# Kernel tuning notes

Measured on AMD Instinct MI355X. Metric: run time of the kernel, lower is better.

The kernel has to match this reference:

```python
import jax, jax.numpy as jnp
import numpy as np

N_NODES = 20000
N_EDGES = 320000
L = 512   # input feature dim (size_dict['small'][0])
D = 256   # hidden dim (feat_channel), heads=1 so head_dim = 256
C = 2     # n_classes


def setup_inputs() -> dict:
    key = jax.random.key(0)
    ks = jax.random.split(key, 18)
    s = 0.02
    inp = {
        "x": jax.random.normal(ks[0], (N_NODES, L), jnp.float32),
        "edge_index": jax.random.randint(ks[1], (2, N_EDGES), 0, N_NODES, dtype=jnp.int32),
        "label": 1,
        # TransformerConv(L, D, heads=1): query/key/value + root skip projections
        "Wq": jax.random.normal(ks[2], (L, D), jnp.float32) * s,
        "bq": jax.random.normal(ks[3], (D,), jnp.float32) * s,
        "Wk": jax.random.normal(ks[4], (L, D), jnp.float32) * s,
        "bk": jax.random.normal(ks[5], (D,), jnp.float32) * s,
        "Wv": jax.random.normal(ks[6], (L, D), jnp.float32) * s,
        "bv": jax.random.normal(ks[7], (D,), jnp.float32) * s,
        "Ws": jax.random.normal(ks[8], (L, D), jnp.float32) * s,
        "bs": jax.random.normal(ks[9], (D,), jnp.float32) * s,
        # GlobalAdaptPooling: tanh-MLP attention (heads = n_classes) + per-class classifier
        "Wa1": jax.random.normal(ks[10], (D, D), jnp.float32) * s,
        "ba1": jax.random.normal(ks[11], (D,), jnp.float32) * s,
        "Wa2": jax.random.normal(ks[12], (D, C), jnp.float32) * s,
        "ba2": jax.random.normal(ks[13], (C,), jnp.float32) * s,
        "Wc": jax.random.normal(ks[14], (C, D), jnp.float32) * s,
        "bc": jax.random.normal(ks[15], (C,), jnp.float32) * s,
    }
    return inp


def _forward(x, edge_index, label, Wq, bq, Wk, bk, Wv, bv, Ws, bs, Wa1, ba1, Wa2, ba2, Wc, bc):
    n = x.shape[0]
    src = edge_index[0]  # message source j
    dst = edge_index[1]  # message target i
    # --- TransformerConv (heads=1, concat, root_weight=True) ---
    q = x @ Wq + bq                      # [N, D]
    k = x @ Wk + bk
    v = x @ Wv + bv
    score = jnp.sum(q[dst] * k[src], axis=-1) / jnp.sqrt(jnp.float32(D))  # [E]
    # segment softmax over incoming edges of each target node
    m = jax.ops.segment_max(score, dst, num_segments=n)
    e = jnp.exp(score - m[dst])
    den = jax.ops.segment_sum(e, dst, num_segments=n)
    alpha = e / den[dst]                 # [E]
    agg = jax.ops.segment_sum(alpha[:, None] * v[src], dst, num_segments=n)  # [N, D]
    h = agg + x @ Ws + bs
    # --- act: GELU (torch exact/erf) ---
    h = jax.nn.gelu(h, approximate=False)
    # --- GlobalAdaptPooling: node attention with n_classes heads ---
    scores = jnp.tanh(h @ Wa1 + ba1) @ Wa2 + ba2      # [N, C]
    attn = jax.nn.softmax(scores, axis=0)             # softmax over nodes
    M = attn.T @ h                                    # [C, D] per-class bag embedding
    logits = (jnp.sum(M * Wc, axis=1) + bc)[None, :]  # [1, C]
    Y_prob = jax.nn.softmax(logits, axis=1)
    A = attn[:, label]                                # [N] attention for target class
    return logits, Y_prob, A


def reference(x, edge_index, label, Wq, bq, Wk, bk, Wv, bv, Ws, bs, Wa1, ba1, Wa2, ba2, Wc, bc):
    return _forward(x, edge_index, label, Wq, bq, Wk, bk, Wv, bv, Ws, bs, Wa1, ba1, Wa2, ba2, Wc, bc)
```

## Files before the change

kernel.cpp:

```cpp
#include <hip/hip_runtime.h>
#include <hip/hip_bf16.h>
#include <math.h>

typedef float f32x4_t __attribute__((ext_vector_type(4)));
typedef float f32x2_t __attribute__((ext_vector_type(2)));
typedef __bf16 bf16x8_t __attribute__((ext_vector_type(8)));

__device__ __forceinline__ float bf2f(unsigned int u){
  union { float f; unsigned int i; } x; x.i = u << 16; return x.f;
}
__device__ __forceinline__ unsigned short f2bf(float f){
  unsigned int x = __float_as_uint(f);
  unsigned int r = (x + 0x7fffu + ((x >> 16) & 1u)) >> 16;
  return (unsigned short)r;
}
__device__ __forceinline__ unsigned int pk2bf(float a, float b){
  return (unsigned int)f2bf(a) | ((unsigned int)f2bf(b) << 16);
}
__device__ __forceinline__ int swz4(int r){ return (r ^ (r >> 2) ^ (r >> 4)) & 3; }

__device__ __forceinline__ void unp8s(uint4 w, float* f, float s){
  f[0] = bf2f(w.x & 0xffffu) * s; f[1] = bf2f(w.x >> 16) * s;
  f[2] = bf2f(w.y & 0xffffu) * s; f[3] = bf2f(w.y >> 16) * s;
  f[4] = bf2f(w.z & 0xffffu) * s; f[5] = bf2f(w.z >> 16) * s;
  f[6] = bf2f(w.w & 0xffffu) * s; f[7] = bf2f(w.w >> 16) * s;
}
__device__ __forceinline__ void unpf8(unsigned int w, float* f){
  f32x2_t lo = __builtin_amdgcn_cvt_pk_f32_fp8(w, false);
  f32x2_t hi = __builtin_amdgcn_cvt_pk_f32_fp8(w, true);
  f[0] = lo[0]; f[1] = lo[1]; f[2] = hi[0]; f[3] = hi[1];
}

#define GLOAD16(gsrc, ldst) \
  __builtin_amdgcn_global_load_lds((const __attribute__((address_space(1))) unsigned int*)(gsrc), \
                                   (__attribute__((address_space(3))) unsigned int*)(ldst), 16, 0, 0)

__global__ void zero_buf(uint4* __restrict__ p, int n16){
  int i = blockIdx.x * 256 + threadIdx.x;
  if (i < n16) p[i] = make_uint4(0, 0, 0, 0);
}

__global__ void prep(const float* __restrict__ x,
                     const float* __restrict__ Wq, const float* __restrict__ Wk,
                     const float* __restrict__ Wv, const float* __restrict__ Ws,
                     const float* __restrict__ bq, const float* __restrict__ bk,
                     const float* __restrict__ bv, const float* __restrict__ bs,
                     const float* __restrict__ Wa1, const int* __restrict__ ei,
                     unsigned short* __restrict__ xbf, unsigned short* __restrict__ wcatT,
                     float* __restrict__ bcat, unsigned short* __restrict__ wa1T,
                     int* __restrict__ deg, int n, int ne, int nbcv){
  const int b = blockIdx.x, tid = threadIdx.x;
  if (b < 2048){
    int idx = b * 256 + tid;
    int c = idx >> 9, k = idx & 511;
    int sel = c >> 8, cc = c & 255;
    const float* W = (sel == 0) ? Wq : (sel == 1) ? Wk : (sel == 2) ? Wv : Ws;
    int p = ((k >> 3) & 3) ^ swz4(c & 127);
    int dst = c * 512 + (k & ~31) + p * 8 + (k & 7);
    wcatT[dst] = f2bf(W[k * 256 + cc]);
    if (idx < 1024){
      int sel2 = idx >> 8, cc2 = idx & 255;
      const float* B = (sel2 == 0) ? bq : (sel2 == 1) ? bk : (sel2 == 2) ? bv : bs;
      bcat[idx] = B[cc2];
    }
  } else if (b < 2304){
    int idx = (b - 2048) * 256 + tid;
    int c = idx >> 8, k = idx & 255;
    wa1T[idx] = f2bf(Wa1[k * 256 + c]);
  } else if (b < 2304 + nbcv){
    int idx = (b - 2304) * 256 + tid;
    if (idx < n * 64){
      int node = idx >> 6, un = idx & 63;
      int k0 = (un >> 2) * 32, u = un & 3;
      const float* src = x + (size_t)node * 512 + k0 + u * 8;
      float4 f0 = *reinterpret_cast<const float4*>(src);
      float4 f1 = *reinterpret_cast<const float4*>(src + 4);
      uint4 o;
      o.x = pk2bf(f0.x, f0.y); o.y = pk2bf(f0.z, f0.w);
      o.z = pk2bf(f1.x, f1.y); o.w = pk2bf(f1.z, f1.w);
      int p = u ^ swz4(node & 127);
      *reinterpret_cast<uint4*>(xbf + (size_t)node * 512 + k0 + p * 8) = o;
    }
  } else {
    int i = (b - 2304 - nbcv) * 256 + tid;
    if (i < ne) atomicAdd(&deg[ei[ne + i]], 1);
  }
}

__global__ __launch_bounds__(256) void gemm_qkvs(const unsigned short* __restrict__ xbf,
                                                 const unsigned short* __restrict__ wcatT,
                                                 const float* __restrict__ bcat,
                                                 unsigned short* __restrict__ qbf,
                                                 unsigned short* __restrict__ sbf,
                                                 unsigned char* __restrict__ kv8,
                                                 int n_nodes, int mblocks){
  __shared__ __align__(16) unsigned char smem[49152];
  const int tid = threadIdx.x;
  const int lane = tid & 63, wave = tid >> 6;
  const int wm = wave >> 1, wn = wave & 1;
  const int g = (blockIdx.x & 7) * mblocks + (blockIdx.x >> 3);
  const int m_blk = g >> 3, n_blk = g & 7;
  const int m0 = m_blk * 128, n0 = n_blk * 128;
  const int lrow = lane >> 2;
  const int lcol = (lane & 3) * 8;
  const int rA0 = min(m0 + wave * 16 + lrow, n_nodes - 1);
  const int rA1 = min(m0 + (wave + 4) * 16 + lrow, n_nodes - 1);
  const int rB0 = n0 + wave * 16 + lrow;
  const int rB1 = rB0 + 64;
  const int r = lane & 15, q4 = lane >> 4;
  const unsigned short* aG0 = xbf   + (size_t)rA0 * 512 + lcol;
  const unsigned short* aG1 = xbf   + (size_t)rA1 * 512 + lcol;
  const unsigned short* bG0 = wcatT + (size_t)rB0 * 512 + lcol;
  const unsigned short* bG1 = wcatT + (size_t)rB1 * 512 + lcol;
  int aoff[4], boff[4];
  #pragma unroll
  for (int mi = 0; mi < 4; mi++){ int rr = wm * 64 + mi * 16 + r; aoff[mi] = rr * 32 + ((q4 ^ swz4(rr)) * 8); }
  #pragma unroll
  for (int ni = 0; ni < 4; ni++){ int rb = wn * 64 + ni * 16 + r; boff[ni] = rb * 32 + ((q4 ^ swz4(rb)) * 8); }
  f32x4_t acc[4][4] = {};
#define STAGE(base, k0) { \
    unsigned short* As_ = (unsigned short*)(smem + (base)); \
    unsigned short* Bs_ = (unsigned short*)(smem + (base) + 8192); \
    GLOAD16(aG0 + (k0), &As_[wave * 512]); \
    GLOAD16(aG1 + (k0), &As_[(wave + 4) * 512]); \
    GLOAD16(bG0 + (k0), &Bs_[wave * 512]); \
    GLOAD16(bG1 + (k0), &Bs_[(wave + 4) * 512]); \
  }
  STAGE(0, 0);
  STAGE(16384, 32);
  int cbase = 0;
  int sbase = 32768;
  for (int t = 0; t < 16; t++){
    if (t + 2 < 16){
      STAGE(sbase, (t + 2) * 32);
      asm volatile("s_waitcnt vmcnt(8)" ::: "memory");
    } else if (t + 1 < 16){
      asm volatile("s_waitcnt vmcnt(4)" ::: "memory");
    } else {
      asm volatile("s_waitcnt vmcnt(0)" ::: "memory");
    }
    __builtin_amdgcn_s_barrier();
    asm volatile("" ::: "memory");
    const unsigned short* As = (const unsigned short*)(smem + cbase);
    const unsigned short* Bs = (const unsigned short*)(smem + cbase + 8192);
    bf16x8_t a[4], b[4];
    #pragma unroll
    for (int mi = 0; mi < 4; mi++) a[mi] = *reinterpret_cast<const bf16x8_t*>(&As[aoff[mi]]);
    #pragma unroll
    for (int ni = 0; ni < 4; ni++) b[ni] = *reinterpret_cast<const bf16x8_t*>(&Bs[boff[ni]]);
    #pragma unroll
    for (int mi = 0; mi < 4; mi++)
      #pragma unroll
      for (int ni = 0; ni < 4; ni++)
        acc[mi][ni] = __builtin_amdgcn_mfma_f32_16x16x32_bf16(b[ni], a[mi], acc[mi][ni], 0, 0, 0);
    __builtin_amdgcn_s_barrier();
    asm volatile("" ::: "memory");
    cbase += 16384; if (cbase == 49152) cbase = 0;
    sbase += 16384; if (sbase == 49152) sbase = 0;
  }
#undef STAGE
  const bool isQ = (n_blk < 2), isS = (n_blk >= 6);
  if (isQ || isS){
    unsigned short* St = (unsigned short*)smem;
    unsigned short* outp = isQ ? qbf : sbf;
    const int colhalf = isQ ? n_blk : (n_blk - 6);
    #pragma unroll
    for (int ch = 0; ch < 2; ch++){
      if (wm == ch){
        #pragma unroll
        for (int mi = 0; mi < 4; mi++){
          #pragma unroll
          for (int ni = 0; ni < 4; ni++){
            int mloc = mi * 16 + r;
            int nl = wn * 64 + ni * 16 + q4 * 4;
            float4 bb = *reinterpret_cast<const float4*>(&bcat[n0 + nl]);
            uint2 w;
            w.x = pk2bf(acc[mi][ni][0] + bb.x, acc[mi][ni][1] + bb.y);
            w.y = pk2bf(acc[mi][ni][2] + bb.z, acc[mi][ni][3] + bb.w);
            *reinterpret_cast<uint2*>(&St[mloc * 152 + nl]) = w;
          }
        }
      }
      __syncthreads();
      #pragma unroll
      for (int it = 0; it < 4; it++){
        int u = it * 256 + tid;
        int row = u >> 4, seg = (u & 15) * 8;
        int node = m0 + ch * 64 + row;
        if (node < n_nodes){
          uint4 v = *reinterpret_cast<const uint4*>(&St[row * 152 + seg]);
          *reinterpret_cast<uint4*>(outp + (size_t)node * 256 + colhalf * 128 + seg) = v;
        }
      }
      __syncthreads();
    }
  } else {
    unsigned char* St8 = smem;
    #pragma unroll
    for (int ch = 0; ch < 2; ch++){
      if (wm == ch){
        #pragma unroll
        for (int mi = 0; mi < 4; mi++){
          #pragma unroll
          for (int ni = 0; ni < 4; ni++){
            int mloc = mi * 16 + r;
            int nl = wn * 64 + ni * 16 + q4 * 4;
            float4 bb = *reinterpret_cast<const float4*>(&bcat[n0 + nl]);
            int u = 0;
            u = __builtin_amdgcn_cvt_pk_fp8_f32(acc[mi][ni][0] + bb.x, acc[mi][ni][1] + bb.y, u, false);
            u = __builtin_amdgcn_cvt_pk_fp8_f32(acc[mi][ni][2] + bb.z, acc[mi][ni][3] + bb.w, u, true);
            *reinterpret_cast<unsigned int*>(&St8[mloc * 144 + nl]) = (unsigned int)u;
          }
        }
      }
      __syncthreads();
      #pragma unroll
      for (int it = 0; it < 2; it++){
        int u = it * 256 + tid;
        int row = u >> 3, seg = (u & 7) * 16;
        int node = m0 + ch * 64 + row;
        if (node < n_nodes){
          uint4 v = *reinterpret_cast<const uint4*>(&St8[row * 144 + seg]);
          *reinterpret_cast<uint4*>(kv8 + (size_t)node * 512 + (n_blk - 2) * 128 + seg) = v;
        }
      }
      __syncthreads();
    }
  }
}

__global__ void scan_deg(const int* __restrict__ deg, int* __restrict__ rowstart, int n, int ne){
  __shared__ int sm[1024];
  int tid = threadIdx.x;
  int per = (n + 1023) / 1024;
  int start = tid * per;
  int sum = 0;
  for (int i = 0; i < per; i++){
    int idx = start + i;
    sum += (idx < n) ? deg[idx] : 0;
  }
  sm[tid] = sum; __syncthreads();
  for (int off = 1; off < 1024; off <<= 1){
    int t = (tid >= off) ? sm[tid - off] : 0;
    __syncthreads();
    sm[tid] += t;
    __syncthreads();
  }
  int run = sm[tid] - sum;
  for (int i = 0; i < per; i++){
    int idx = start + i;
    if (idx < n){
      rowstart[idx] = run;
      run += deg[idx];
    }
  }
  if (tid == 0) rowstart[n] = ne;
}

__global__ void scatter_edges(const int* __restrict__ ei, const int* __restrict__ rowstart,
                              int* __restrict__ cursor, int* __restrict__ csrsrc, int ne){
  int i = blockIdx.x * 256 + threadIdx.x;
  if (i < ne){
    int d = ei[ne + i];
    int pos = atomicAdd(&cursor[d], 1);
    csrsrc[rowstart[d] + pos] = ei[i] << 9;
  }
}

__global__ __launch_bounds__(256) void edge_attn(const unsigned short* __restrict__ qbf,
                                                 const unsigned short* __restrict__ sbf,
                                                 const unsigned char* __restrict__ kv8,
                                                 const int* __restrict__ rowstart,
                                                 const int* __restrict__ csrsrc,
                                                 unsigned short* __restrict__ hbf, int n_nodes){
  const int tid = threadIdx.x;
  const int lane = tid & 63, wave = tid >> 6;
  const int g = lane >> 4, t = lane & 15;
  const int chain = g;
  const int node = blockIdx.x * 4 + wave;
  const bool active = node < n_nodes;
  const int nd = active ? node : 0;
  const float qs = 0.0625f * 1.44269504088896340736f;
  float q[16];
  {
    const unsigned short* qp = qbf + (size_t)nd * 256 + t * 16;
    uint4 w0 = *reinterpret_cast<const uint4*>(qp);
    uint4 w1 = *reinterpret_cast<const uint4*>(qp + 8);
    unp8s(w0, q, qs); unp8s(w1, q + 8, qs);
  }
  int rs = rowstart[nd];
  int re = active ? rowstart[nd + 1] : rs;
  float m = -1e30f, den = 0.f;
  float acc[16];
  #pragma unroll
  for (int j = 0; j < 16; j++) acc[j] = 0.f;
  const int i0 = rs + chain;
  uint4 kA = make_uint4(0,0,0,0), vA = kA, kB = kA, vB = kA;
  if (i0 < re){
    const unsigned char* p1 = kv8 + (size_t)csrsrc[i0] + t * 16;
    kA = *reinterpret_cast<const uint4*>(p1);
    vA = *reinterpret_cast<const uint4*>(p1 + 256);
    if (i0 + 4 < re){
      const unsigned char* p2 = kv8 + (size_t)csrsrc[i0 + 4] + t * 16;
      kB = *reinterpret_cast<const uint4*>(p2);
      vB = *reinterpret_cast<const uint4*>(p2 + 256);
    }
  }
  for (int i = i0; i < re; i += 8){
    uint4 k1 = kA, v1 = vA, k2 = kB, v2 = vB;
    const bool has2 = (i + 4 < re);
    if (i + 8 < re){
      const unsigned char* p1 = kv8 + (size_t)csrsrc[i + 8] + t * 16;
      kA = *reinterpret_cast<const uint4*>(p1);
      vA = *reinterpret_cast<const uint4*>(p1 + 256);
      if (i + 12 < re){
        const unsigned char* p2 = kv8 + (size_t)csrsrc[i + 12] + t * 16;
        kB = *reinterpret_cast<const uint4*>(p2);
        vB = *reinterpret_cast<const uint4*>(p2 + 256);
      }
    }
    float kf1[16], kf2[16];
    unpf8(k1.x, kf1); unpf8(k1.y, kf1 + 4); unpf8(k1.z, kf1 + 8); unpf8(k1.w, kf1 + 12);
    unpf8(k2.x, kf2); unpf8(k2.y, kf2 + 4); unpf8(k2.z, kf2 + 8); unpf8(k2.w, kf2 + 12);
    float s1 = 0.f, s2 = 0.f;
    #pragma unroll
    for (int j = 0; j < 16; j++){ s1 = fmaf(q[j], kf1[j], s1); s2 = fmaf(q[j], kf2[j], s2); }
    s1 += __shfl_xor(s1, 1); s2 += __shfl_xor(s2, 1);
    s1 += __shfl_xor(s1, 2); s2 += __shfl_xor(s2, 2);
    s1 += __shfl_xor(s1, 4); s2 += __shfl_xor(s2, 4);
    s1 += __shfl_xor(s1, 8); s2 += __shfl_xor(s2, 8);
    if (!has2) s2 = -1e30f;
    float vf1[16], vf2[16];
    unpf8(v1.x, vf1); unpf8(v1.y, vf1 + 4); unpf8(v1.z, vf1 + 8); unpf8(v1.w, vf1 + 12);
    unpf8(v2.x, vf2); unpf8(v2.y, vf2 + 4); unpf8(v2.z, vf2 + 8); unpf8(v2.w, vf2 + 12);
    float mn = fmaxf(m, fmaxf(s1, s2));
    float sc = exp2f(m - mn);
    float e1 = exp2f(s1 - mn);
    float e2 = exp2f(s2 - mn);
    den = den * sc + e1 + e2;
    #pragma unroll
    for (int j = 0; j < 16; j++)
      acc[j] = fmaf(acc[j], sc, fmaf(e1, vf1[j], e2 * vf2[j]));
    m = mn;
  }
  #pragma unroll
  for (int step = 16; step <= 32; step <<= 1){
    float mo  = __shfl_xor(m, step);
    float dno = __shfl_xor(den, step);
    float mn  = fmaxf(m, mo);
    float a_  = exp2f(m - mn);
    float b_  = exp2f(mo - mn);
    den = den * a_ + dno * b_;
    #pragma unroll
    for (int j = 0; j < 16; j++){
      float oth = __shfl_xor(acc[j], step);
      acc[j] = acc[j] * a_ + oth * b_;
    }
    m = mn;
  }
  float inv = (den > 0.f) ? 1.f / den : 0.f;
  const unsigned short* sp = sbf + (size_t)nd * 256 + t * 16;
  uint4 s0 = *reinterpret_cast<const uint4*>(sp);
  uint4 s1v = *reinterpret_cast<const uint4*>(sp + 8);
  float sf[16]; unp8s(s0, sf, 1.0f); unp8s(s1v, sf + 8, 1.0f);
  const float inv_sqrt2 = 0.70710678118654752f;
  unsigned int o[8];
  #pragma unroll
  for (int j = 0; j < 8; j++){
    float h0 = acc[2 * j] * inv + sf[2 * j];
    float h1 = acc[2 * j + 1] * inv + sf[2 * j + 1];
    h0 = 0.5f * h0 * (1.f + erff(h0 * inv_sqrt2));
    h1 = 0.5f * h1 * (1.f + erff(h1 * inv_sqrt2));
    o[j] = (unsigned int)f2bf(h0) | ((unsigned int)f2bf(h1) << 16);
  }
  if (active && g == 0){
    uint4* dst = reinterpret_cast<uint4*>(hbf + (size_t)node * 256 + t * 16);
    dst[0] = make_uint4(o[0], o[1], o[2], o[3]);
    dst[1] = make_uint4(o[4], o[5], o[6], o[7]);
  }
}

__global__ __launch_bounds__(256) void mlp_mfma(const unsigned short* __restrict__ hbf,
                                                const unsigned short* __restrict__ wa1T,
                                                const float* __restrict__ ba1,
                                                const float* __restrict__ Wa2,
                                                const float* __restrict__ ba2,
                                                float* __restrict__ s2, int n_nodes){
  __shared__ __align__(16) unsigned short As[64 * 72];
  __shared__ float s2s[64][2];
  const int tid = threadIdx.x;
  const int lane = tid & 63, wave = tid >> 6;
  const int m0 = blockIdx.x * 64;
  const int c0 = wave * 64;
  const int r = lane & 15, rg = (lane >> 4) * 4;
  if (tid < 128) s2s[tid >> 1][tid & 1] = 0.f;
  f32x4_t acc[4][4] = {};
  for (int k0 = 0; k0 < 256; k0 += 64){
    int arow = tid >> 2, akc = (tid & 3) * 16;
    uint4 a0v = make_uint4(0,0,0,0), a1v = make_uint4(0,0,0,0);
    if (m0 + arow < n_nodes){
      const unsigned short* src = hbf + (size_t)(m0 + arow) * 256 + k0 + akc;
      a0v = *reinterpret_cast<const uint4*>(src);
      a1v = *reinterpret_cast<const uint4*>(src + 8);
    }
    *reinterpret_cast<uint4*>(&As[arow * 72 + akc]) = a0v;
    *reinterpret_cast<uint4*>(&As[arow * 72 + akc + 8]) = a1v;
    __syncthreads();
    #pragma unroll
    for (int kk = 0; kk < 2; kk++){
      int kg = kk * 32 + (lane >> 4) * 8;
      bf16x8_t a[4], b[4];
      #pragma unroll
      for (int mi = 0; mi < 4; mi++)
        a[mi] = *reinterpret_cast<const bf16x8_t*>(&As[(mi * 16 + r) * 72 + kg]);
      #pragma unroll
      for (int ni = 0; ni < 4; ni++)
        b[ni] = *reinterpret_cast<const bf16x8_t*>(wa1T + (size_t)(c0 + ni * 16 + r) * 256 + k0 + kg);
      #pragma unroll
      for (int mi = 0; mi < 4; mi++)
        #pragma unroll
        for (int ni = 0; ni < 4; ni++)
          acc[mi][ni] = __builtin_amdgcn_mfma_f32_16x16x32_bf16(a[mi], b[ni], acc[mi][ni], 0, 0, 0);
    }
    __syncthreads();
  }
  float w20[4], w21[4], b1c[4];
  #pragma unroll
  for (int ni = 0; ni < 4; ni++){
    int col = c0 + ni * 16 + r;
    w20[ni] = Wa2[col * 2]; w21[ni] = Wa2[col * 2 + 1]; b1c[ni] = ba1[col];
  }
  #pragma unroll
  for (int mi = 0; mi < 4; mi++){
    #pragma unroll
    for (int j = 0; j < 4; j++){
      float t0 = 0.f, t1 = 0.f;
      #pragma unroll
      for (int ni = 0; ni < 4; ni++){
        float t = tanhf(acc[mi][ni][j] + b1c[ni]);
        t0 += t * w20[ni]; t1 += t * w21[ni];
      }
      t0 += __shfl_xor(t0, 1); t0 += __shfl_xor(t0, 2);
      t0 += __shfl_xor(t0, 4); t0 += __shfl_xor(t0, 8);
      t1 += __shfl_xor(t1, 1); t1 += __shfl_xor(t1, 2);
      t1 += __shfl_xor(t1, 4); t1 += __shfl_xor(t1, 8);
      if (r == 0){
        int row = mi * 16 + rg + j;
        atomicAdd(&s2s[row][0], t0);
        atomicAdd(&s2s[row][1], t1);
      }
    }
  }
  __syncthreads();
  if (tid < 128){
    int row = tid >> 1, c = tid & 1;
    int node = m0 + row;
    if (node < n_nodes) s2[node * 2 + c] = s2s[row][c] + ba2[c];
  }
}

__global__ void col_reduce(const float* __restrict__ s2, float* __restrict__ red, int n){
  __shared__ float sm[1024];
  __shared__ float mshare[2];
  int tid = threadIdx.x;
  float mx0 = -INFINITY, mx1 = -INFINITY;
  for (int i = tid; i < n; i += 1024){
    mx0 = fmaxf(mx0, s2[2 * i]);
    mx1 = fmaxf(mx1, s2[2 * i + 1]);
  }
  sm[tid] = mx0; __syncthreads();
  for (int off = 512; off > 0; off >>= 1){
    if (tid < off) sm[tid] = fmaxf(sm[tid], sm[tid + off]);
    __syncthreads();
  }
  if (tid == 0) mshare[0] = sm[0];
  __syncthreads();
  sm[tid] = mx1; __syncthreads();
  for (int off = 512; off > 0; off >>= 1){
    if (tid < off) sm[tid] = fmaxf(sm[tid], sm[tid + off]);
    __syncthreads();
  }
  if (tid == 0) mshare[1] = sm[0];
  __syncthreads();
  float m0 = mshare[0], m1 = mshare[1];
  float s0 = 0.f, s1 = 0.f;
  for (int i = tid; i < n; i += 1024){
    s0 += expf(s2[2 * i] - m0);
    s1 += expf(s2[2 * i + 1] - m1);
  }
  sm[tid] = s0; __syncthreads();
  for (int off = 512; off > 0; off >>= 1){
    if (tid < off) sm[tid] += sm[tid + off];
    __syncthreads();
  }
  float den0 = sm[0];
  __syncthreads();
  sm[tid] = s1; __syncthreads();
  for (int off = 512; off > 0; off >>= 1){
    if (tid < off) sm[tid] += sm[tid + off];
    __syncthreads();
  }
  if (tid == 0){
    red[0] = m0; red[1] = m1; red[2] = den0; red[3] = sm[0];
  }
}

__global__ __launch_bounds__(256) void attn_M(const float* __restrict__ s2, const float* __restrict__ red,
                                              const unsigned short* __restrict__ hbf, const int* __restrict__ label,
                                              float* __restrict__ Mbuf, float* __restrict__ outA, int n){
  __shared__ float a0s[256], a1s[256];
  __shared__ float Ms[512];
  int tid = threadIdx.x;
  int n0 = blockIdx.x * 256;
  int node = n0 + tid;
  float m0 = red[0], m1 = red[1];
  float i0 = 1.f / red[2], i1 = 1.f / red[3];
  float a0 = 0.f, a1 = 0.f;
  if (node < n){
    a0 = expf(s2[2 * node] - m0) * i0;
    a1 = expf(s2[2 * node + 1] - m1) * i1;
    outA[node] = (label[0] == 0) ? a0 : a1;
  }
  a0s[tid] = a0; a1s[tid] = a1;
  Ms[tid] = 0.f; Ms[tid + 256] = 0.f;
  __syncthreads();
  const int dgrp = tid & 31;
  const int nl = tid >> 5;
  float M0[8] = {}, M1[8] = {};
  for (int i = nl; i < 256; i += 8){
    int nd = n0 + i;
    if (nd >= n) break;
    uint4 w = *reinterpret_cast<const uint4*>(hbf + (size_t)nd * 256 + dgrp * 8);
    float f[8]; unp8s(w, f, 1.0f);
    float A0 = a0s[i], A1 = a1s[i];
    #pragma unroll
    for (int j = 0; j < 8; j++){
      M0[j] = fmaf(A0, f[j], M0[j]);
      M1[j] = fmaf(A1, f[j], M1[j]);
    }
  }
  #pragma unroll
  for (int j = 0; j < 8; j++){
    M0[j] += __shfl_xor(M0[j], 32);
    M1[j] += __shfl_xor(M1[j], 32);
  }
  if ((tid & 32) == 0){
    #pragma unroll
    for (int j = 0; j < 8; j++){
      atomicAdd(&Ms[dgrp * 8 + j], M0[j]);
      atomicAdd(&Ms[256 + dgrp * 8 + j], M1[j]);
    }
  }
  __syncthreads();
  atomicAdd(&Mbuf[tid], Ms[tid]);
  atomicAdd(&Mbuf[256 + tid], Ms[tid + 256]);
}

__global__ void final_k(const float* __restrict__ Mbuf, const float* __restrict__ Wc,
                        const float* __restrict__ bc, float* __restrict__ out){
  __shared__ float sm[256];
  __shared__ float l0s;
  int tid = threadIdx.x;
  float p0 = Mbuf[tid] * Wc[tid];
  float p1 = Mbuf[256 + tid] * Wc[256 + tid];
  sm[tid] = p0; __syncthreads();
  for (int off = 128; off > 0; off >>= 1){
    if (tid < off) sm[tid] += sm[tid + off];
    __syncthreads();
  }
  if (tid == 0) l0s = sm[0];
  __syncthreads();
  sm[tid] = p1; __syncthreads();
  for (int off = 128; off > 0; off >>= 1){
    if (tid < off) sm[tid] += sm[tid + off];
    __syncthreads();
  }
  if (tid == 0){
    float l0 = l0s + bc[0];
    float l1 = sm[0] + bc[1];
    out[0] = l0; out[1] = l1;
    float mx = fmaxf(l0, l1);
    float e0 = expf(l0 - mx), e1 = expf(l1 - mx);
    float inv = 1.f / (e0 + e1);
    out[2] = e0 * inv; out[3] = e1 * inv;
  }
}

extern "C" void kernel_launch(void* const* d_in, const int* in_sizes, int n_in,
                              void* d_out, int out_size, void* d_ws, size_t ws_size,
                              hipStream_t stream) {
  const float* x   = (const float*)d_in[0];
  const int*   ei  = (const int*)d_in[1];
  const int*   lab = (const int*)d_in[2];
  const float* Wq  = (const float*)d_in[3];
  const float* bq  = (const float*)d_in[4];
  const float* Wk  = (const float*)d_in[5];
  const float* bk  = (const float*)d_in[6];
  const float* Wv  = (const float*)d_in[7];
  const float* bv  = (const float*)d_in[8];
  const float* Ws  = (const float*)d_in[9];
  const float* bs  = (const float*)d_in[10];
  const float* Wa1 = (const float*)d_in[11];
  const float* ba1 = (const float*)d_in[12];
  const float* Wa2 = (const float*)d_in[13];
  const float* ba2 = (const float*)d_in[14];
  const float* Wc  = (const float*)d_in[15];
  const float* bc  = (const float*)d_in[16];
  float* out = (float*)d_out;

  const int n  = in_sizes[0] / 512;
  const int ne = in_sizes[1] / 2;

  char* ws = (char*)d_ws;
  size_t off = 0;
  auto take = [&](size_t bytes){ size_t r = off; off += (bytes + 255) & ~(size_t)255; return r; };
  unsigned short* wcatT  = (unsigned short*)(ws + take((size_t)1024 * 512 * 2));
  float*          bcat   = (float*)(ws + take(1024 * 4));
  unsigned short* xbf    = (unsigned short*)(ws + take((size_t)n * 512 * 2));
  unsigned short* qbf    = (unsigned short*)(ws + take((size_t)n * 256 * 2));
  unsigned short* sbf    = (unsigned short*)(ws + take((size_t)n * 256 * 2));
  unsigned char*  kv8    = (unsigned char*)(ws + take((size_t)n * 512));
  unsigned short* hbf    = (unsigned short*)(ws + take((size_t)n * 256 * 2));
  unsigned short* wa1T   = (unsigned short*)(ws + take((size_t)256 * 256 * 2));
  float*          s2     = (float*)(ws + take((size_t)n * 2 * 4));
  size_t zoff = off;
  int*            deg    = (int*)(ws + take((size_t)n * 4));
  int*            cursor = (int*)(ws + take((size_t)n * 4));
  float*          Mbuf   = (float*)(ws + take(512 * 4));
  size_t zlen = off - zoff;
  int*            rowst  = (int*)(ws + take((size_t)(n + 1) * 4));
  int*            csrsrc = (int*)(ws + take((size_t)ne * 4));
  float*          red    = (float*)(ws + take(4 * 4));

  const int z16 = (int)(zlen / 16);
  zero_buf<<<(z16 + 255) / 256, 256, 0, stream>>>((uint4*)(ws + zoff), z16);

  const int nbcv = (n * 64 + 255) / 256;
  const int nbdh = (ne + 255) / 256;
  prep<<<2304 + nbcv + nbdh, 256, 0, stream>>>(x, Wq, Wk, Wv, Ws, bq, bk, bv, bs, Wa1, ei,
                                               xbf, wcatT, bcat, wa1T, deg, n, ne, nbcv);
  const int mblocks = (n + 127) / 128;
  gemm_qkvs<<<8 * mblocks, 256, 0, stream>>>(xbf, wcatT, bcat, qbf, sbf, kv8, n, mblocks);
  scan_deg<<<1, 1024, 0, stream>>>(deg, rowst, n, ne);
  scatter_edges<<<(ne + 255) / 256, 256, 0, stream>>>(ei, rowst, cursor, csrsrc, ne);
  edge_attn<<<(n + 3) / 4, 256, 0, stream>>>(qbf, sbf, kv8, rowst, csrsrc, hbf, n);
  mlp_mfma<<<(n + 63) / 64, 256, 0, stream>>>(hbf, wa1T, ba1, Wa2, ba2, s2, n);
  col_reduce<<<1, 1024, 0, stream>>>(s2, red, n);
  attn_M<<<(n + 255) / 256, 256, 0, stream>>>(s2, red, hbf, lab, Mbuf, out + 4, n);
  final_k<<<1, 256, 0, stream>>>(Mbuf, Wc, bc, out);
  (void)ws_size; (void)out_size; (void)n_in;
}
```

Before: 200.2 us.

## Store keys as fp16 with fdot2 scoring, two nodes per wave, fast GELU/tanh

Keys are now written by the projection GEMM as fp16 into a separate buffer, while values stay fp8 in their own buffer. Edge scores use packed fp16 dot products (fdot2) with the query converted to fp16. The edge-attention kernel now maps two nodes per wave with two chains each, up from one node with four chains. Exact erf GELU and tanhf are replaced with exp2-based approximations. This aims to cut fp8 unpack ALU work and improve per-node parallelism, at the cost of doubling key gather bytes and adding approximation error in the activations.

```diff
diff --git a/kernel.cpp b/kernel.cpp
--- a/kernel.cpp
+++ b/kernel.cpp
@@ -5,6 +5,13 @@
 typedef float f32x4_t __attribute__((ext_vector_type(4)));
 typedef float f32x2_t __attribute__((ext_vector_type(2)));
 typedef __bf16 bf16x8_t __attribute__((ext_vector_type(8)));
+typedef _Float16 h2_t __attribute__((ext_vector_type(2)));
+
+#if defined(__has_builtin)
+#if __has_builtin(__builtin_amdgcn_fdot2)
+#define HAS_FDOT2 1
+#endif
+#endif
 
 __device__ __forceinline__ float bf2f(unsigned int u){
   union { float f; unsigned int i; } x; x.i = u << 16; return x.f;
@@ -16,6 +23,11 @@
 }
 __device__ __forceinline__ unsigned int pk2bf(float a, float b){
   return (unsigned int)f2bf(a) | ((unsigned int)f2bf(b) << 16);
+}
+__device__ __forceinline__ unsigned int pk2h(float a, float b){
+  auto p = __builtin_amdgcn_cvt_pkrtz(a, b);
+  union { decltype(p) v; unsigned int u; } c; c.v = p;
+  return c.u;
 }
 __device__ __forceinline__ int swz4(int r){ return (r ^ (r >> 2) ^ (r >> 4)) & 3; }
 
@@ -29,6 +41,36 @@
   f32x2_t lo = __builtin_amdgcn_cvt_pk_f32_fp8(w, false);
   f32x2_t hi = __builtin_amdgcn_cvt_pk_f32_fp8(w, true);
   f[0] = lo[0]; f[1] = lo[1]; f[2] = hi[0]; f[3] = hi[1];
+}
+__device__ __forceinline__ float fast_tanh(float y){
+  float e = exp2f(y * 2.8853901817f);
+  return 1.0f - 2.0f / (e + 1.0f);
+}
+__device__ __forceinline__ float fast_gelu(float x){
+  float x2 = x * x;
+  float u = x * fmaf(0.1029527f, x2, 2.3022339f);
+  float e = exp2f(u);
+  return x - x / (e + 1.0f);
+}
+__device__ __forceinline__ float dot16f16(const uint4& a, const uint4& b, const h2_t* qh){
+  float s = 0.f;
+#ifdef HAS_FDOT2
+  const h2_t* ka = reinterpret_cast<const h2_t*>(&a);
+  const h2_t* kb = reinterpret_cast<const h2_t*>(&b);
+  #pragma unroll
+  for (int j = 0; j < 4; j++) s = __builtin_amdgcn_fdot2(ka[j], qh[j], s, false);
+  #pragma unroll
+  for (int j = 0; j < 4; j++) s = __builtin_amdgcn_fdot2(kb[j], qh[4 + j], s, false);
+#else
+  const _Float16* ka = reinterpret_cast<const _Float16*>(&a);
+  const _Float16* kb = reinterpret_cast<const _Float16*>(&b);
+  const _Float16* qq = reinterpret_cast<const _Float16*>(qh);
+  #pragma unroll
+  for (int j = 0; j < 8; j++) s = fmaf((float)ka[j], (float)qq[j], s);
+  #pragma unroll
+  for (int j = 0; j < 8; j++) s = fmaf((float)kb[j], (float)qq[8 + j], s);
+#endif
+  return s;
 }
 
 #define GLOAD16(gsrc, ldst) \
@@ -92,7 +134,8 @@
                                                  const float* __restrict__ bcat,
                                                  unsigned short* __restrict__ qbf,
                                                  unsigned short* __restrict__ sbf,
-                                                 unsigned char* __restrict__ kv8,
+                                                 unsigned short* __restrict__ k16,
+                                                 unsigned char* __restrict__ v8,
                                                  int n_nodes, int mblocks){
   __shared__ __align__(16) unsigned char smem[49152];
   const int tid = threadIdx.x;
@@ -159,11 +202,13 @@
     sbase += 16384; if (sbase == 49152) sbase = 0;
   }
 #undef STAGE
-  const bool isQ = (n_blk < 2), isS = (n_blk >= 6);
-  if (isQ || isS){
+  const bool isV = (n_blk == 4 || n_blk == 5);
+  if (!isV){
     unsigned short* St = (unsigned short*)smem;
-    unsigned short* outp = isQ ? qbf : sbf;
-    const int colhalf = isQ ? n_blk : (n_blk - 6);
+    unsigned short* outp; int colhalf; bool asF16 = false;
+    if (n_blk < 2){ outp = qbf; colhalf = n_blk; }
+    else if (n_blk < 4){ outp = k16; colhalf = n_blk - 2; asF16 = true; }
+    else { outp = sbf; colhalf = n_blk - 6; }
     #pragma unroll
     for (int ch = 0; ch < 2; ch++){
       if (wm == ch){
@@ -175,8 +220,13 @@
             int nl = wn * 64 + ni * 16 + q4 * 4;
             float4 bb = *reinterpret_cast<const float4*>(&bcat[n0 + nl]);
             uint2 w;
-            w.x = pk2bf(acc[mi][ni][0] + bb.x, acc[mi][ni][1] + bb.y);
-            w.y = pk2bf(acc[mi][ni][2] + bb.z, acc[mi][ni][3] + bb.w);
+            if (asF16){
+              w.x = pk2h(acc[mi][ni][0] + bb.x, acc[mi][ni][1] + bb.y);
+              w.y = pk2h(acc[mi][ni][2] + bb.z, acc[mi][ni][3] + bb.w);
+            } else {
+              w.x = pk2bf(acc[mi][ni][0] + bb.x, acc[mi][ni][1] + bb.y);
+              w.y = pk2bf(acc[mi][ni][2] + bb.z, acc[mi][ni][3] + bb.w);
+            }
             *reinterpret_cast<uint2*>(&St[mloc * 152 + nl]) = w;
           }
         }
@@ -221,7 +271,7 @@
         int node = m0 + ch * 64 + row;
         if (node < n_nodes){
           uint4 v = *reinterpret_cast<const uint4*>(&St8[row * 144 + seg]);
-          *reinterpret_cast<uint4*>(kv8 + (size_t)node * 512 + (n_blk - 2) * 128 + seg) = v;
+          *reinterpret_cast<uint4*>(v8 + (size_t)node * 256 + (n_blk - 4) * 128 + seg) = v;
         }
       }
       __syncthreads();
@@ -263,30 +313,36 @@
   if (i < ne){
     int d = ei[ne + i];
     int pos = atomicAdd(&cursor[d], 1);
-    csrsrc[rowstart[d] + pos] = ei[i] << 9;
+    csrsrc[rowstart[d] + pos] = ei[i];
   }
 }
 
 __global__ __launch_bounds__(256) void edge_attn(const unsigned short* __restrict__ qbf,
                                                  const unsigned short* __restrict__ sbf,
-                                                 const unsigned char* __restrict__ kv8,
+                                                 const unsigned short* __restrict__ k16,
+                                                 const unsigned char* __restrict__ v8,
                                                  const int* __restrict__ rowstart,
                                                  const int* __restrict__ csrsrc,
                                                  unsigned short* __restrict__ hbf, int n_nodes){
   const int tid = threadIdx.x;
   const int lane = tid & 63, wave = tid >> 6;
   const int g = lane >> 4, t = lane & 15;
-  const int chain = g;
-  const int node = blockIdx.x * 4 + wave;
+  const int chain = g & 1;
+  const int node = blockIdx.x * 8 + wave * 2 + (g >> 1);
   const bool active = node < n_nodes;
   const int nd = active ? node : 0;
   const float qs = 0.0625f * 1.44269504088896340736f;
-  float q[16];
+  h2_t qh[8];
   {
     const unsigned short* qp = qbf + (size_t)nd * 256 + t * 16;
     uint4 w0 = *reinterpret_cast<const uint4*>(qp);
     uint4 w1 = *reinterpret_cast<const uint4*>(qp + 8);
-    unp8s(w0, q, qs); unp8s(w1, q + 8, qs);
+    float qf[16]; unp8s(w0, qf, qs); unp8s(w1, qf + 8, qs);
+    #pragma unroll
+    for (int j = 0; j < 8; j++){
+      h2_t v; v[0] = (_Float16)qf[2 * j]; v[1] = (_Float16)qf[2 * j + 1];
+      qh[j] = v;
+    }
   }
   int rs = rowstart[nd];
   int re = active ? rowstart[nd + 1] : rs;
@@ -295,44 +351,35 @@
   #pragma unroll
   for (int j = 0; j < 16; j++) acc[j] = 0.f;
   const int i0 = rs + chain;
-  uint4 kA = make_uint4(0,0,0,0), vA = kA, kB = kA, vB = kA;
+  uint4 kA0 = make_uint4(0,0,0,0), kA1 = kA0, vA = kA0, kB0 = kA0, kB1 = kA0, vB = kA0;
+#define LOADE(idx, K0, K1, V) { \
+    int src_ = csrsrc[idx]; \
+    const unsigned short* kp_ = k16 + (size_t)src_ * 256 + t * 16; \
+    K0 = *reinterpret_cast<const uint4*>(kp_); \
+    K1 = *reinterpret_cast<const uint4*>(kp_ + 8); \
+    V  = *reinterpret_cast<const uint4*>(v8 + (size_t)src_ * 256 + t * 16); \
+  }
   if (i0 < re){
-    const unsigned char* p1 = kv8 + (size_t)csrsrc[i0] + t * 16;
-    kA = *reinterpret_cast<const uint4*>(p1);
-    vA = *reinterpret_cast<const uint4*>(p1 + 256);
-    if (i0 + 4 < re){
-      const unsigned char* p2 = kv8 + (size_t)csrsrc[i0 + 4] + t * 16;
-      kB = *reinterpret_cast<const uint4*>(p2);
-      vB = *reinterpret_cast<const uint4*>(p2 + 256);
-    }
-  }
-  for (int i = i0; i < re; i += 8){
-    uint4 k1 = kA, v1 = vA, k2 = kB, v2 = vB;
-    const bool has2 = (i + 4 < re);
-    if (i + 8 < re){
-      const unsigned char* p1 = kv8 + (size_t)csrsrc[i + 8] + t * 16;
-      kA = *reinterpret_cast<const uint4*>(p1);
-      vA = *reinterpret_cast<const uint4*>(p1 + 256);
-      if (i + 12 < re){
-        const unsigned char* p2 = kv8 + (size_t)csrsrc[i + 12] + t * 16;
-        kB = *reinterpret_cast<const uint4*>(p2);
-        vB = *reinterpret_cast<const uint4*>(p2 + 256);
-      }
-    }
-    float kf1[16], kf2[16];
-    unpf8(k1.x, kf1); unpf8(k1.y, kf1 + 4); unpf8(k1.z, kf1 + 8); unpf8(k1.w, kf1 + 12);
-    unpf8(k2.x, kf2); unpf8(k2.y, kf2 + 4); unpf8(k2.z, kf2 + 8); unpf8(k2.w, kf2 + 12);
-    float s1 = 0.f, s2 = 0.f;
-    #pragma unroll
-    for (int j = 0; j < 16; j++){ s1 = fmaf(q[j], kf1[j], s1); s2 = fmaf(q[j], kf2[j], s2); }
+    LOADE(i0, kA0, kA1, vA);
+    if (i0 + 2 < re) LOADE(i0 + 2, kB0, kB1, vB);
+  }
+  for (int i = i0; i < re; i += 4){
+    uint4 x10 = kA0, x11 = kA1, xv1 = vA, x20 = kB0, x21 = kB1, xv2 = vB;
+    const bool has2 = (i + 2 < re);
+    if (i + 4 < re){
+      LOADE(i + 4, kA0, kA1, vA);
+      if (i + 6 < re) LOADE(i + 6, kB0, kB1, vB);
+    }
+    float s1 = dot16f16(x10, x11, qh);
+    float s2 = dot16f16(x20, x21, qh);
     s1 += __shfl_xor(s1, 1); s2 += __shfl_xor(s2, 1);
     s1 += __shfl_xor(s1, 2); s2 += __shfl_xor(s2, 2);
     s1 += __shfl_xor(s1, 4); s2 += __shfl_xor(s2, 4);
     s1 += __shfl_xor(s1, 8); s2 += __shfl_xor(s2, 8);
     if (!has2) s2 = -1e30f;
     float vf1[16], vf2[16];
-    unpf8(v1.x, vf1); unpf8(v1.y, vf1 + 4); unpf8(v1.z, vf1 + 8); unpf8(v1.w, vf1 + 12);
-    unpf8(v2.x, vf2); unpf8(v2.y, vf2 + 4); unpf8(v2.z, vf2 + 8); unpf8(v2.w, vf2 + 12);
+    unpf8(xv1.x, vf1); unpf8(xv1.y, vf1 + 4); unpf8(xv1.z, vf1 + 8); unpf8(xv1.w, vf1 + 12);
+    unpf8(xv2.x, vf2); unpf8(xv2.y, vf2 + 4); unpf8(xv2.z, vf2 + 8); unpf8(xv2.w, vf2 + 12);
     float mn = fmaxf(m, fmaxf(s1, s2));
     float sc = exp2f(m - mn);
     float e1 = exp2f(s1 - mn);
@@ -343,37 +390,33 @@
       acc[j] = fmaf(acc[j], sc, fmaf(e1, vf1[j], e2 * vf2[j]));
     m = mn;
   }
-  #pragma unroll
-  for (int step = 16; step <= 32; step <<= 1){
-    float mo  = __shfl_xor(m, step);
-    float dno = __shfl_xor(den, step);
+#undef LOADE
+  {
+    float mo  = __shfl_xor(m, 16);
+    float dno = __shfl_xor(den, 16);
     float mn  = fmaxf(m, mo);
     float a_  = exp2f(m - mn);
     float b_  = exp2f(mo - mn);
     den = den * a_ + dno * b_;
     #pragma unroll
     for (int j = 0; j < 16; j++){
-      float oth = __shfl_xor(acc[j], step);
+      float oth = __shfl_xor(acc[j], 16);
       acc[j] = acc[j] * a_ + oth * b_;
     }
-    m = mn;
   }
   float inv = (den > 0.f) ? 1.f / den : 0.f;
   const unsigned short* sp = sbf + (size_t)nd * 256 + t * 16;
   uint4 s0 = *reinterpret_cast<const uint4*>(sp);
   uint4 s1v = *reinterpret_cast<const uint4*>(sp + 8);
   float sf[16]; unp8s(s0, sf, 1.0f); unp8s(s1v, sf + 8, 1.0f);
-  const float inv_sqrt2 = 0.70710678118654752f;
   unsigned int o[8];
   #pragma unroll
   for (int j = 0; j < 8; j++){
-    float h0 = acc[2 * j] * inv + sf[2 * j];
-    float h1 = acc[2 * j + 1] * inv + sf[2 * j + 1];
-    h0 = 0.5f * h0 * (1.f + erff(h0 * inv_sqrt2));
-    h1 = 0.5f * h1 * (1.f + erff(h1 * inv_sqrt2));
+    float h0 = fast_gelu(acc[2 * j] * inv + sf[2 * j]);
+    float h1 = fast_gelu(acc[2 * j + 1] * inv + sf[2 * j + 1]);
     o[j] = (unsigned int)f2bf(h0) | ((unsigned int)f2bf(h1) << 16);
   }
-  if (active && g == 0){
+  if (active && chain == 0){
     uint4* dst = reinterpret_cast<uint4*>(hbf + (size_t)node * 256 + t * 16);
     dst[0] = make_uint4(o[0], o[1], o[2], o[3]);
     dst[1] = make_uint4(o[4], o[5], o[6], o[7]);
@@ -437,7 +480,7 @@
       float t0 = 0.f, t1 = 0.f;
       #pragma unroll
       for (int ni = 0; ni < 4; ni++){
-        float t = tanhf(acc[mi][ni][j] + b1c[ni]);
+        float t = fast_tanh(acc[mi][ni][j] + b1c[ni]);
         t0 += t * w20[ni]; t1 += t * w21[ni];
       }
       t0 += __shfl_xor(t0, 1); t0 += __shfl_xor(t0, 2);
@@ -619,7 +662,8 @@
   unsigned short* xbf    = (unsigned short*)(ws + take((size_t)n * 512 * 2));
   unsigned short* qbf    = (unsigned short*)(ws + take((size_t)n * 256 * 2));
   unsigned short* sbf    = (unsigned short*)(ws + take((size_t)n * 256 * 2));
-  unsigned char*  kv8    = (unsigned char*)(ws + take((size_t)n * 512));
+  unsigned short* k16    = (unsigned short*)(ws + take((size_t)n * 256 * 2));
+  unsigned char*  v8     = (unsigned char*)(ws + take((size_t)n * 256));
   unsigned short* hbf    = (unsigned short*)(ws + take((size_t)n * 256 * 2));
   unsigned short* wa1T   = (unsigned short*)(ws + take((size_t)256 * 256 * 2));
   float*          s2     = (float*)(ws + take((size_t)n * 2 * 4));
@@ -640,10 +684,10 @@
   prep<<<2304 + nbcv + nbdh, 256, 0, stream>>>(x, Wq, Wk, Wv, Ws, bq, bk, bv, bs, Wa1, ei,
                                                xbf, wcatT, bcat, wa1T, deg, n, ne, nbcv);
   const int mblocks = (n + 127) / 128;
-  gemm_qkvs<<<8 * mblocks, 256, 0, stream>>>(xbf, wcatT, bcat, qbf, sbf, kv8, n, mblocks);
+  gemm_qkvs<<<8 * mblocks, 256, 0, stream>>>(xbf, wcatT, bcat, qbf, sbf, k16, v8, n, mblocks);
   scan_deg<<<1, 1024, 0, stream>>>(deg, rowst, n, ne);
   scatter_edges<<<(ne + 255) / 256, 256, 0, stream>>>(ei, rowst, cursor, csrsrc, ne);
-  edge_attn<<<(n + 3) / 4, 256, 0, stream>>>(qbf, sbf, kv8, rowst, csrsrc, hbf, n);
+  edge_attn<<<(n + 7) / 8, 256, 0, stream>>>(qbf, sbf, k16, v8, rowst, csrsrc, hbf, n);
   mlp_mfma<<<(n + 63) / 64, 256, 0, stream>>>(hbf, wa1T, ba1, Wa2, ba2, s2, n);
   col_reduce<<<1, 1024, 0, stream>>>(s2, red, n);
   attn_M<<<(n + 255) / 256, 256, 0, stream>>>(s2, red, hbf, lab, Mbuf, out + 4, n);
```

Measured after the change: 206.9 us. 3.4% more time.

## Process two nodes per wave in edge attention and use fast GELU/tanh approximations

Applied to the files above, without the earlier changes.

The edge attention kernel now maps two destination nodes to each wave, with two chains per node instead of four. This halves the block count and drops one cross-lane merge step, which should help because average degree is about 16. The exact erf GELU is replaced by a tanh-form GELU built on exp2, and tanhf in the pooling MLP by an exp2-based formula. The GELU is now the tanh approximation rather than the exact erf form, so it is less accurate, and each node has less memory-level parallelism.

```diff
diff --git a/kernel.cpp b/kernel.cpp
--- a/kernel.cpp
+++ b/kernel.cpp
@@ -29,6 +29,16 @@
   f32x2_t lo = __builtin_amdgcn_cvt_pk_f32_fp8(w, false);
   f32x2_t hi = __builtin_amdgcn_cvt_pk_f32_fp8(w, true);
   f[0] = lo[0]; f[1] = lo[1]; f[2] = hi[0]; f[3] = hi[1];
+}
+__device__ __forceinline__ float fast_tanh(float y){
+  float e = exp2f(y * 2.8853901817f);
+  return 1.0f - 2.0f / (e + 1.0f);
+}
+__device__ __forceinline__ float fast_gelu(float x){
+  float x2 = x * x;
+  float u = x * fmaf(0.1029527f, x2, 2.3022339f);
+  float e = exp2f(u);
+  return x - x / (e + 1.0f);
 }
 
 #define GLOAD16(gsrc, ldst) \
@@ -276,8 +286,8 @@
   const int tid = threadIdx.x;
   const int lane = tid & 63, wave = tid >> 6;
   const int g = lane >> 4, t = lane & 15;
-  const int chain = g;
-  const int node = blockIdx.x * 4 + wave;
+  const int chain = g & 1;
+  const int node = blockIdx.x * 8 + wave * 2 + (g >> 1);
   const bool active = node < n_nodes;
   const int nd = active ? node : 0;
   const float qs = 0.0625f * 1.44269504088896340736f;
@@ -300,21 +310,21 @@
     const unsigned char* p1 = kv8 + (size_t)csrsrc[i0] + t * 16;
     kA = *reinterpret_cast<const uint4*>(p1);
     vA = *reinterpret_cast<const uint4*>(p1 + 256);
-    if (i0 + 4 < re){
-      const unsigned char* p2 = kv8 + (size_t)csrsrc[i0 + 4] + t * 16;
+    if (i0 + 2 < re){
+      const unsigned char* p2 = kv8 + (size_t)csrsrc[i0 + 2] + t * 16;
       kB = *reinterpret_cast<const uint4*>(p2);
       vB = *reinterpret_cast<const uint4*>(p2 + 256);
     }
   }
-  for (int i = i0; i < re; i += 8){
+  for (int i = i0; i < re; i += 4){
     uint4 k1 = kA, v1 = vA, k2 = kB, v2 = vB;
-    const bool has2 = (i + 4 < re);
-    if (i + 8 < re){
-      const unsigned char* p1 = kv8 + (size_t)csrsrc[i + 8] + t * 16;
+    const bool has2 = (i + 2 < re);
+    if (i + 4 < re){
+      const unsigned char* p1 = kv8 + (size_t)csrsrc[i + 4] + t * 16;
       kA = *reinterpret_cast<const uint4*>(p1);
       vA = *reinterpret_cast<const uint4*>(p1 + 256);
-      if (i + 12 < re){
-        const unsigned char* p2 = kv8 + (size_t)csrsrc[i + 12] + t * 16;
+      if (i + 6 < re){
+        const unsigned char* p2 = kv8 + (size_t)csrsrc[i + 6] + t * 16;
         kB = *reinterpret_cast<const uint4*>(p2);
         vB = *reinterpret_cast<const uint4*>(p2 + 256);
       }
@@ -343,37 +353,32 @@
       acc[j] = fmaf(acc[j], sc, fmaf(e1, vf1[j], e2 * vf2[j]));
     m = mn;
   }
-  #pragma unroll
-  for (int step = 16; step <= 32; step <<= 1){
-    float mo  = __shfl_xor(m, step);
-    float dno = __shfl_xor(den, step);
+  {
+    float mo  = __shfl_xor(m, 16);
+    float dno = __shfl_xor(den, 16);
     float mn  = fmaxf(m, mo);
     float a_  = exp2f(m - mn);
     float b_  = exp2f(mo - mn);
     den = den * a_ + dno * b_;
     #pragma unroll
     for (int j = 0; j < 16; j++){
-      float oth = __shfl_xor(acc[j], step);
+      float oth = __shfl_xor(acc[j], 16);
       acc[j] = acc[j] * a_ + oth * b_;
     }
-    m = mn;
   }
   float inv = (den > 0.f) ? 1.f / den : 0.f;
   const unsigned short* sp = sbf + (size_t)nd * 256 + t * 16;
   uint4 s0 = *reinterpret_cast<const uint4*>(sp);
   uint4 s1v = *reinterpret_cast<const uint4*>(sp + 8);
   float sf[16]; unp8s(s0, sf, 1.0f); unp8s(s1v, sf + 8, 1.0f);
-  const float inv_sqrt2 = 0.70710678118654752f;
   unsigned int o[8];
   #pragma unroll
   for (int j = 0; j < 8; j++){
-    float h0 = acc[2 * j] * inv + sf[2 * j];
-    float h1 = acc[2 * j + 1] * inv + sf[2 * j + 1];
-    h0 = 0.5f * h0 * (1.f + erff(h0 * inv_sqrt2));
-    h1 = 0.5f * h1 * (1.f + erff(h1 * inv_sqrt2));
+    float h0 = fast_gelu(acc[2 * j] * inv + sf[2 * j]);
+    float h1 = fast_gelu(acc[2 * j + 1] * inv + sf[2 * j + 1]);
     o[j] = (unsigned int)f2bf(h0) | ((unsigned int)f2bf(h1) << 16);
   }
-  if (active && g == 0){
+  if (active && chain == 0){
     uint4* dst = reinterpret_cast<uint4*>(hbf + (size_t)node * 256 + t * 16);
     dst[0] = make_uint4(o[0], o[1], o[2], o[3]);
     dst[1] = make_uint4(o[4], o[5], o[6], o[7]);
@@ -437,7 +442,7 @@
       float t0 = 0.f, t1 = 0.f;
       #pragma unroll
       for (int ni = 0; ni < 4; ni++){
-        float t = tanhf(acc[mi][ni][j] + b1c[ni]);
+        float t = fast_tanh(acc[mi][ni][j] + b1c[ni]);
         t0 += t * w20[ni]; t1 += t * w21[ni];
       }
       t0 += __shfl_xor(t0, 1); t0 += __shfl_xor(t0, 2);
@@ -643,7 +648,7 @@
   gemm_qkvs<<<8 * mblocks, 256, 0, stream>>>(xbf, wcatT, bcat, qbf, sbf, kv8, n, mblocks);
   scan_deg<<<1, 1024, 0, stream>>>(deg, rowst, n, ne);
   scatter_edges<<<(ne + 255) / 256, 256, 0, stream>>>(ei, rowst, cursor, csrsrc, ne);
-  edge_attn<<<(n + 3) / 4, 256, 0, stream>>>(qbf, sbf, kv8, rowst, csrsrc, hbf, n);
+  edge_attn<<<(n + 7) / 8, 256, 0, stream>>>(qbf, sbf, kv8, rowst, csrsrc, hbf, n);
   mlp_mfma<<<(n + 63) / 64, 256, 0, stream>>>(hbf, wa1T, ba1, Wa2, ba2, s2, n);
   col_reduce<<<1, 1024, 0, stream>>>(s2, red, n);
   attn_M<<<(n + 255) / 256, 256, 0, stream>>>(s2, red, hbf, lab, Mbuf, out + 4, n);
```

Measured after the change: 197.5 us. Within noise of the previous version (-1.4%).
